# Performance work log

Hardware: AMD Instinct MI355X
Metric: run time of the kernel (lower is better)

## Reference

```python
import jax, jax.numpy as jnp
import numpy as np

EPS = 1e-8  # torch F.cosine_similarity norm clamp


def setup_inputs() -> dict:
    key = jax.random.key(0)
    ks = jax.random.split(key, 5)
    B, H, C, S, CS, K = 256, 256, 16384, 64, 32, 8
    query = jax.random.normal(ks[0], (B, H), dtype=jnp.float32)
    episode_embeddings = jax.random.normal(ks[1], (C, H), dtype=jnp.float32)
    episodes = jax.random.normal(ks[2], (C, S, H), dtype=jnp.float32)
    compressed_episodes = jax.random.normal(ks[3], (C, CS, H), dtype=jnp.float32)
    is_compressed = jax.random.randint(ks[4], (C,), 0, 2) == 1
    return {
        "query": query,
        "episode_embeddings": episode_embeddings,
        "episodes": episodes,
        "compressed_episodes": compressed_episodes,
        "is_compressed": is_compressed,
        "k": K,
    }


def reference(query, episode_embeddings, episodes, compressed_episodes, is_compressed, k):
    # cosine similarity  [B, C]
    qn = query / jnp.maximum(jnp.linalg.norm(query, axis=-1, keepdims=True), EPS)
    en = episode_embeddings / jnp.maximum(
        jnp.linalg.norm(episode_embeddings, axis=-1, keepdims=True), EPS)
    sim = qn @ en.T
    top_scores, top_idx = jax.lax.top_k(sim, k)  # [B, k]

    S = episodes.shape[1]
    CS = compressed_episodes.shape[1]
    full = episodes[top_idx]                # [B, k, S, H] gather
    comp = compressed_episodes[top_idx]     # [B, k, CS, H] gather
    comp_padded = jnp.pad(comp, ((0, 0), (0, 0), (0, S - CS), (0, 0)))
    flag = is_compressed[top_idx][..., None, None]  # [B, k, 1, 1]
    retrieved = jnp.where(flag, comp_padded, full)  # [B, k, S, H]
    return retrieved, top_scores
```

## Files before the change

### kernel.cpp

```cpp
#include <hip/hip_runtime.h>
#include <math.h>

#define B_  256
#define H_  256
#define C_  16384
#define S_  64
#define CS_ 32
#define K_  8
#define EPS 1e-8f
#define RET_ ((size_t)B_ * K_ * S_ * H_)

typedef __attribute__((ext_vector_type(8))) short short8v;
typedef __attribute__((ext_vector_type(4))) float f32x4;


__device__ inline unsigned short f2bf(float f) {
    unsigned u = __builtin_bit_cast(unsigned, f);
    unsigned r = u + 0x7fffu + ((u >> 16) & 1u);
    return (unsigned short)(r >> 16);
}
__device__ inline unsigned ordf(float f) {
    unsigned u = __builtin_bit_cast(unsigned, f);
    return u ^ ((u >> 31) ? 0xFFFFFFFFu : 0x80000000u);
}
__device__ inline short8v pack8(float4 a, float4 b) {
    short8v r;
    r[0] = (short)f2bf(a.x); r[1] = (short)f2bf(a.y);
    r[2] = (short)f2bf(a.z); r[3] = (short)f2bf(a.w);
    r[4] = (short)f2bf(b.x); r[5] = (short)f2bf(b.y);
    r[6] = (short)f2bf(b.z); r[7] = (short)f2bf(b.w);
    return r;
}
__device__ inline void ce(unsigned long long& a, unsigned long long& b) {
    unsigned long long lo = a < b ? a : b;
    a = a < b ? b : a;
    b = lo;
}
__device__ inline void merge_shfl(unsigned long long best[8], int xorlane) {
    unsigned long long m[8];
    #pragma unroll
    for (int i = 0; i < 8; ++i) {
        unsigned long long p = __shfl_xor(best[7 - i], xorlane);
        m[i] = best[i] > p ? best[i] : p;
    }
    ce(m[0], m[4]); ce(m[1], m[5]); ce(m[2], m[6]); ce(m[3], m[7]);
    ce(m[0], m[2]); ce(m[1], m[3]); ce(m[4], m[6]); ce(m[5], m[7]);
    ce(m[0], m[1]); ce(m[2], m[3]); ce(m[4], m[5]); ce(m[6], m[7]);
    #pragma unroll
    for (int i = 0; i < 8; ++i) best[i] = m[i];
}

#define LSTR 40
__global__ __launch_bounds__(256) void simsel_kernel(const float* __restrict__ q,
                                                     const float* __restrict__ e,
                                                     const unsigned* __restrict__ icw,
                                                     unsigned long long* __restrict__ candbuf,
                                                     int* __restrict__ mode) {
    const int t = threadIdx.x;
    if (blockIdx.x == 1024) {
        __shared__ int f;
        if (t == 0) f = 0;
        __syncthreads();
        int any = 0;
        for (int i = t; i < 4096; i += 256)
            if (icw[i] & 0xFFFFFF00u) any = 1;
        if (any) atomicOr(&f, 1);
        __syncthreads();
        if (t == 0) *mode = f;
        return;
    }

    __shared__ union {
        struct { unsigned short Qs[64 * LSTR]; unsigned short Es[64 * LSTR]; } st;
        float tile[64 * 65];
    } sm;
    __shared__ float einv_s[64];
    const int lane = t & 63, wv = t >> 6;
    const int wm = wv >> 1, wn = wv & 1;
    const int bid = blockIdx.x;
    const int ct = (bid & 7) * 32 + (bid >> 5);
    const int bt = (bid >> 3) & 3;
    const int c0 = ct * 64, b0 = bt * 64;
    const int r = t >> 2, g = t & 3;
    const float4* q4 = (const float4*)q;
    const float4* e4 = (const float4*)e;

    float esq = 0.f;
    f32x4 acc[2][2];
    #pragma unroll
    for (int i = 0; i < 2; ++i)
        #pragma unroll
        for (int j = 0; j < 2; ++j) acc[i][j] = (f32x4){0.f, 0.f, 0.f, 0.f};

    for (int hc = 0; hc < 8; ++hc) {
        __syncthreads();
        float4 a0 = q4[(size_t)(b0 + r) * 64 + hc * 8 + g * 2];
        float4 a1 = q4[(size_t)(b0 + r) * 64 + hc * 8 + g * 2 + 1];
        float4 e0 = e4[(size_t)(c0 + r) * 64 + hc * 8 + g * 2];
        float4 e1 = e4[(size_t)(c0 + r) * 64 + hc * 8 + g * 2 + 1];
        esq += e0.x * e0.x + e0.y * e0.y + e0.z * e0.z + e0.w * e0.w
             + e1.x * e1.x + e1.y * e1.y + e1.z * e1.z + e1.w * e1.w;
        *(short8v*)&sm.st.Qs[r * LSTR + g * 8] = pack8(a0, a1);
        *(short8v*)&sm.st.Es[r * LSTR + g * 8] = pack8(e0, e1);
        __syncthreads();

        short8v afr[2], bfr[2];
        #pragma unroll
        for (int mi = 0; mi < 2; ++mi)
            afr[mi] = *(short8v*)&sm.st.Qs[(wm * 32 + mi * 16 + (lane & 15)) * LSTR + (lane >> 4) * 8];
        #pragma unroll
        for (int ni = 0; ni < 2; ++ni)
            bfr[ni] = *(short8v*)&sm.st.Es[(wn * 32 + ni * 16 + (lane & 15)) * LSTR + (lane >> 4) * 8];
        #pragma unroll
        for (int mi = 0; mi < 2; ++mi)
            #pragma unroll
            for (int ni = 0; ni < 2; ++ni)
                acc[mi][ni] = __builtin_amdgcn_mfma_f32_16x16x32_bf16(
                    afr[mi], bfr[ni], acc[mi][ni], 0, 0, 0);
    }

    esq += __shfl_xor(esq, 1);
    esq += __shfl_xor(esq, 2);
    if (g == 0) einv_s[r] = 1.0f / fmaxf(sqrtf(esq), EPS);
    __syncthreads();

    #pragma unroll
    for (int mi = 0; mi < 2; ++mi)
        #pragma unroll
        for (int j = 0; j < 4; ++j) {
            int row = wm * 32 + mi * 16 + (lane >> 4) * 4 + j;
            #pragma unroll
            for (int ni = 0; ni < 2; ++ni) {
                int col = wn * 32 + ni * 16 + (lane & 15);
                sm.tile[row * 65 + col] = acc[mi][ni][j] * einv_s[col];
            }
        }
    __syncthreads();

    unsigned long long best[8];
    #pragma unroll
    for (int k = 0; k < 8; ++k) best[k] = 0ull;
    for (int i = 0; i < 16; ++i) {
        int c = g * 16 + i;
        float v = sm.tile[r * 65 + c];
        unsigned long long key = ((unsigned long long)ordf(v) << 32)
                               | (unsigned)(0xFFFFFFFFu - (unsigned)(c0 + c));
        if (key > best[7]) {
            best[7] = key;
            #pragma unroll
            for (int k = 7; k > 0; --k)
                if (best[k] > best[k - 1]) {
                    unsigned long long tmp = best[k];
                    best[k] = best[k - 1]; best[k - 1] = tmp;
                }
        }
    }
    merge_shfl(best, 1);
    merge_shfl(best, 2);
    if (g == 0) {
        #pragma unroll
        for (int k = 0; k < 8; ++k)
            candbuf[(size_t)(b0 + r) * 2048 + ct * 8 + k] = best[k];
    }
}

__global__ __launch_bounds__(256) void merge_kernel(const float* __restrict__ q,
                                                    const float* __restrict__ e,
                                                    const unsigned long long* __restrict__ candbuf,
                                                    float* __restrict__ out_scores,
                                                    int* __restrict__ top_idx) {
    __shared__ unsigned long long wtop[4][32];
    __shared__ unsigned long long sel32[32];
    __shared__ float rs[32];
    __shared__ int   ri[32];
    const int t = threadIdx.x, b = blockIdx.x;
    const int wv = t >> 6, lane = t & 63;

    const unsigned long long* lp = candbuf + (size_t)b * 2048 + (size_t)(wv * 64 + lane) * 8;
    unsigned long long k0 = lp[0], k1 = lp[1], k2 = lp[2], k3 = lp[3],
                       k4 = lp[4], k5 = lp[5], k6 = lp[6], k7 = lp[7];
    int p = 0;
    unsigned long long cur = k0;

    for (int it = 0; it < 32; ++it) {
        unsigned long long km = cur;
        #pragma unroll
        for (int d = 1; d < 64; d <<= 1) {
            unsigned long long o = __shfl_xor(km, d);
            km = o > km ? o : km;
        }
        if (lane == 0) wtop[wv][it] = km;
        if (cur == km) {
            ++p;
            cur = (p == 1) ? k1 : (p == 2) ? k2 : (p == 3) ? k3 : (p == 4) ? k4
                : (p == 5) ? k5 : (p == 6) ? k6 : (p == 7) ? k7 : 0ull;
        }
    }
    __syncthreads();

    if (t == 0) {
        int i0 = 0, i1 = 0, i2 = 0, i3 = 0;
        for (int it = 0; it < 32; ++it) {
            unsigned long long v0 = (i0 < 32) ? wtop[0][i0] : 0ull;
            unsigned long long v1 = (i1 < 32) ? wtop[1][i1] : 0ull;
            unsigned long long v2 = (i2 < 32) ? wtop[2][i2] : 0ull;
            unsigned long long v3 = (i3 < 32) ? wtop[3][i3] : 0ull;
            unsigned long long m01 = v0 > v1 ? v0 : v1;
            unsigned long long m23 = v2 > v3 ? v2 : v3;
            unsigned long long mx  = m01 > m23 ? m01 : m23;
            sel32[it] = mx;
            if (mx == v0) ++i0; else if (mx == v1) ++i1;
            else if (mx == v2) ++i2; else ++i3;
        }
    }
    __syncthreads();

    float4 qv = ((const float4*)q)[(size_t)b * 64 + lane];
    float qsq = qv.x * qv.x + qv.y * qv.y + qv.z * qv.z + qv.w * qv.w;
    #pragma unroll
    for (int d = 1; d < 64; d <<= 1) qsq += __shfl_xor(qsq, d);
    float qi = 1.0f / fmaxf(sqrtf(qsq), EPS);

    for (int m = wv; m < 32; m += 4) {
        int idx = (int)(0xFFFFFFFFu - (unsigned)(sel32[m] & 0xFFFFFFFFull));
        float4 ev = ((const float4*)e)[(size_t)idx * 64 + lane];
        float dot = qv.x * ev.x + qv.y * ev.y + qv.z * ev.z + qv.w * ev.w;
        float ss  = ev.x * ev.x + ev.y * ev.y + ev.z * ev.z + ev.w * ev.w;
        #pragma unroll
        for (int d = 1; d < 64; d <<= 1) {
            dot += __shfl_xor(dot, d);
            ss  += __shfl_xor(ss, d);
        }
        if (lane == 0) {
            rs[m] = dot * qi * (1.0f / fmaxf(sqrtf(ss), EPS));
            ri[m] = idx;
        }
    }
    __syncthreads();

    if (t < 64) {
        float val; int idx, slot;
        if (t < 32) { val = rs[t]; idx = ri[t]; slot = t; }
        else        { val = -INFINITY; idx = 0x7fffffff; slot = -1; }
        for (int pp = 0; pp < 8; ++pp) {
            float bs = val; int bi = idx, bsl = slot;
            #pragma unroll
            for (int d = 1; d < 64; d <<= 1) {
                float os = __shfl_xor(bs, d);
                int   oi = __shfl_xor(bi, d);
                int   osl = __shfl_xor(bsl, d);
                if (os > bs || (os == bs && oi < bi)) { bs = os; bi = oi; bsl = osl; }
            }
            if (t == 0) { out_scores[b * K_ + pp] = bs; top_idx[b * K_ + pp] = bi; }
            if (slot == bsl) val = -INFINITY;
        }
    }
}

__global__ __launch_bounds__(256) void gather_kernel(const float* __restrict__ epi,
                                                     const float* __restrict__ comp,
                                                     const void* __restrict__ icp,
                                                     const int* __restrict__ top_idx,
                                                     const int* __restrict__ mode,
                                                     float* __restrict__ out) {
    const int bj = blockIdx.x;
    const int c = top_idx[bj];
    const int m = *mode;
    const int flag = m ? (((const unsigned char*)icp)[c] != 0)
                       : (((const int*)icp)[c] != 0);
    const int t = threadIdx.x;
    f32x4* o4 = (f32x4*)out + (size_t)bj * 4096;
    if (!flag) {
        const f32x4* s4 = (const f32x4*)epi + (size_t)c * 4096;
        #pragma unroll 4
        for (int i = t; i < 4096; i += 256)
            __builtin_nontemporal_store(__builtin_nontemporal_load(s4 + i), o4 + i);
    } else {
        const f32x4* s4 = (const f32x4*)comp + (size_t)c * 2048;
        #pragma unroll 4
        for (int i = t; i < 2048; i += 256)
            __builtin_nontemporal_store(__builtin_nontemporal_load(s4 + i), o4 + i);
        const f32x4 z = (f32x4){0.f, 0.f, 0.f, 0.f};
        #pragma unroll 4
        for (int i = 2048 + t; i < 4096; i += 256)
            __builtin_nontemporal_store(z, o4 + i);
    }
}

extern "C" void kernel_launch(void* const* d_in, const int* in_sizes, int n_in,
                              void* d_out, int out_size, void* d_ws, size_t ws_size,
                              hipStream_t stream) {
    const float* query = (const float*)d_in[0];
    const float* emb   = (const float*)d_in[1];
    const float* epi   = (const float*)d_in[2];
    const float* comp  = (const float*)d_in[3];
    const void*  icp   = d_in[4];
    float* out = (float*)d_out;

    unsigned long long* candbuf = (unsigned long long*)d_ws;
    int* mode   = (int*)((char*)d_ws + (4u << 20));
    int* topidx = mode + 1;
    float* out_scores = out + RET_;

    simsel_kernel<<<1025, 256, 0, stream>>>(query, emb, (const unsigned*)icp,
                                            candbuf, mode);
    merge_kernel<<<B_, 256, 0, stream>>>(query, emb, candbuf, out_scores, topidx);
    gather_kernel<<<B_ * K_, 256, 0, stream>>>(epi, comp, icp, topidx, mode, out);
}
```

Measured before the change: 107.6 us.

## Fuse merge into gather with redundant per-block selection; double-buffer simsel loads

Merges the top-k merge and gather kernels into one launch in which each (batch, slot) block recomputes the full candidate merge and then copies its selected episode. This removes a kernel launch and the top_idx round trip, at the cost of eight times the merge work and candidate-buffer reads. The similarity kernel now processes 64-wide K chunks with register prefetch of the next chunk, halving the barrier count and overlapping global loads with MFMA work. The shared-memory row stride is widened to fit the larger chunk.

```diff
diff --git a/kernel.cpp b/kernel.cpp
--- a/kernel.cpp
+++ b/kernel.cpp
@@ -50,7 +50,7 @@
     for (int i = 0; i < 8; ++i) best[i] = m[i];
 }
 
-#define LSTR 40
+#define LSTR 72
 __global__ __launch_bounds__(256) void simsel_kernel(const float* __restrict__ q,
                                                      const float* __restrict__ e,
                                                      const unsigned* __restrict__ icw,
@@ -92,31 +92,53 @@
         #pragma unroll
         for (int j = 0; j < 2; ++j) acc[i][j] = (f32x4){0.f, 0.f, 0.f, 0.f};
 
-    for (int hc = 0; hc < 8; ++hc) {
+    float4 qb[2][4], eb[2][4];
+    #pragma unroll
+    for (int u = 0; u < 4; ++u) {
+        qb[0][u] = q4[(size_t)(b0 + r) * 64 + g * 4 + u];
+        eb[0][u] = e4[(size_t)(c0 + r) * 64 + g * 4 + u];
+    }
+
+    #pragma unroll
+    for (int hc = 0; hc < 4; ++hc) {
+        const int cur = hc & 1, nxt = cur ^ 1;
+        #pragma unroll
+        for (int u = 0; u < 4; ++u) {
+            float4 ev = eb[cur][u];
+            esq += ev.x * ev.x + ev.y * ev.y + ev.z * ev.z + ev.w * ev.w;
+        }
+        *(short8v*)&sm.st.Qs[r * LSTR + g * 16]     = pack8(qb[cur][0], qb[cur][1]);
+        *(short8v*)&sm.st.Qs[r * LSTR + g * 16 + 8] = pack8(qb[cur][2], qb[cur][3]);
+        *(short8v*)&sm.st.Es[r * LSTR + g * 16]     = pack8(eb[cur][0], eb[cur][1]);
+        *(short8v*)&sm.st.Es[r * LSTR + g * 16 + 8] = pack8(eb[cur][2], eb[cur][3]);
+        if (hc < 3) {
+            #pragma unroll
+            for (int u = 0; u < 4; ++u) {
+                qb[nxt][u] = q4[(size_t)(b0 + r) * 64 + (hc + 1) * 16 + g * 4 + u];
+                eb[nxt][u] = e4[(size_t)(c0 + r) * 64 + (hc + 1) * 16 + g * 4 + u];
+            }
+        }
         __syncthreads();
-        float4 a0 = q4[(size_t)(b0 + r) * 64 + hc * 8 + g * 2];
-        float4 a1 = q4[(size_t)(b0 + r) * 64 + hc * 8 + g * 2 + 1];
-        float4 e0 = e4[(size_t)(c0 + r) * 64 + hc * 8 + g * 2];
-        float4 e1 = e4[(size_t)(c0 + r) * 64 + hc * 8 + g * 2 + 1];
-        esq += e0.x * e0.x + e0.y * e0.y + e0.z * e0.z + e0.w * e0.w
-             + e1.x * e1.x + e1.y * e1.y + e1.z * e1.z + e1.w * e1.w;
-        *(short8v*)&sm.st.Qs[r * LSTR + g * 8] = pack8(a0, a1);
-        *(short8v*)&sm.st.Es[r * LSTR + g * 8] = pack8(e0, e1);
+
+        #pragma unroll
+        for (int ks = 0; ks < 2; ++ks) {
+            short8v afr[2], bfr[2];
+            #pragma unroll
+            for (int mi = 0; mi < 2; ++mi)
+                afr[mi] = *(short8v*)&sm.st.Qs[(wm * 32 + mi * 16 + (lane & 15)) * LSTR
+                                               + ks * 32 + (lane >> 4) * 8];
+            #pragma unroll
+            for (int ni = 0; ni < 2; ++ni)
+                bfr[ni] = *(short8v*)&sm.st.Es[(wn * 32 + ni * 16 + (lane & 15)) * LSTR
+                                               + ks * 32 + (lane >> 4) * 8];
+            #pragma unroll
+            for (int mi = 0; mi < 2; ++mi)
+                #pragma unroll
+                for (int ni = 0; ni < 2; ++ni)
+                    acc[mi][ni] = __builtin_amdgcn_mfma_f32_16x16x32_bf16(
+                        afr[mi], bfr[ni], acc[mi][ni], 0, 0, 0);
+        }
         __syncthreads();
-
-        short8v afr[2], bfr[2];
-        #pragma unroll
-        for (int mi = 0; mi < 2; ++mi)
-            afr[mi] = *(short8v*)&sm.st.Qs[(wm * 32 + mi * 16 + (lane & 15)) * LSTR + (lane >> 4) * 8];
-        #pragma unroll
-        for (int ni = 0; ni < 2; ++ni)
-            bfr[ni] = *(short8v*)&sm.st.Es[(wn * 32 + ni * 16 + (lane & 15)) * LSTR + (lane >> 4) * 8];
-        #pragma unroll
-        for (int mi = 0; mi < 2; ++mi)
-            #pragma unroll
-            for (int ni = 0; ni < 2; ++ni)
-                acc[mi][ni] = __builtin_amdgcn_mfma_f32_16x16x32_bf16(
-                    afr[mi], bfr[ni], acc[mi][ni], 0, 0, 0);
     }
 
     esq += __shfl_xor(esq, 1);
@@ -164,16 +186,19 @@
     }
 }
 
-__global__ __launch_bounds__(256) void merge_kernel(const float* __restrict__ q,
-                                                    const float* __restrict__ e,
-                                                    const unsigned long long* __restrict__ candbuf,
-                                                    float* __restrict__ out_scores,
-                                                    int* __restrict__ top_idx) {
+__global__ __launch_bounds__(256) void merge_gather_kernel(
+        const float* __restrict__ q, const float* __restrict__ e,
+        const unsigned long long* __restrict__ candbuf,
+        const void* __restrict__ icp, const int* __restrict__ mode,
+        const float* __restrict__ epi, const float* __restrict__ comp,
+        float* __restrict__ out, float* __restrict__ out_scores) {
     __shared__ unsigned long long wtop[4][32];
     __shared__ unsigned long long sel32[32];
     __shared__ float rs[32];
     __shared__ int   ri[32];
-    const int t = threadIdx.x, b = blockIdx.x;
+    __shared__ int   sel_c;
+    const int t = threadIdx.x;
+    const int j = blockIdx.x >> 8, b = blockIdx.x & 255;
     const int wv = t >> 6, lane = t & 63;
 
     const unsigned long long* lp = candbuf + (size_t)b * 2048 + (size_t)(wv * 64 + lane) * 8;
@@ -251,25 +276,17 @@
                 int   osl = __shfl_xor(bsl, d);
                 if (os > bs || (os == bs && oi < bi)) { bs = os; bi = oi; bsl = osl; }
             }
-            if (t == 0) { out_scores[b * K_ + pp] = bs; top_idx[b * K_ + pp] = bi; }
+            if (t == 0 && pp == j) { out_scores[b * K_ + j] = bs; sel_c = bi; }
             if (slot == bsl) val = -INFINITY;
         }
     }
-}
-
-__global__ __launch_bounds__(256) void gather_kernel(const float* __restrict__ epi,
-                                                     const float* __restrict__ comp,
-                                                     const void* __restrict__ icp,
-                                                     const int* __restrict__ top_idx,
-                                                     const int* __restrict__ mode,
-                                                     float* __restrict__ out) {
-    const int bj = blockIdx.x;
-    const int c = top_idx[bj];
-    const int m = *mode;
-    const int flag = m ? (((const unsigned char*)icp)[c] != 0)
-                       : (((const int*)icp)[c] != 0);
-    const int t = threadIdx.x;
-    f32x4* o4 = (f32x4*)out + (size_t)bj * 4096;
+    __syncthreads();
+
+    const int c = sel_c;
+    const int m_ = *mode;
+    const int flag = m_ ? (((const unsigned char*)icp)[c] != 0)
+                        : (((const int*)icp)[c] != 0);
+    f32x4* o4 = (f32x4*)out + ((size_t)b * K_ + j) * 4096;
     if (!flag) {
         const f32x4* s4 = (const f32x4*)epi + (size_t)c * 4096;
         #pragma unroll 4
@@ -298,12 +315,11 @@
     float* out = (float*)d_out;
 
     unsigned long long* candbuf = (unsigned long long*)d_ws;
-    int* mode   = (int*)((char*)d_ws + (4u << 20));
-    int* topidx = mode + 1;
+    int* mode = (int*)((char*)d_ws + (4u << 20));
     float* out_scores = out + RET_;
 
     simsel_kernel<<<1025, 256, 0, stream>>>(query, emb, (const unsigned*)icp,
                                             candbuf, mode);
-    merge_kernel<<<B_, 256, 0, stream>>>(query, emb, candbuf, out_scores, topidx);
-    gather_kernel<<<B_ * K_, 256, 0, stream>>>(epi, comp, icp, topidx, mode, out);
-}
+    merge_gather_kernel<<<B_ * K_, 256, 0, stream>>>(query, emb, candbuf, icp, mode,
+                                                     epi, comp, out, out_scores);
+}
```

New measurement: 121.8 us. 1.13x slower.

## Double-buffer similarity GEMM smem tiles and parallelize top-k merge with bitonic shuffles

Applied to the files above, without the earlier changes.

The similarity kernel now double-buffers the Q and E shared-memory tiles. The next H-chunk is prefetched into registers while MFMAs run on the current one, which removes one barrier per iteration. In the merge kernel, the serial single-thread 4-way merge of per-wave top-32 lists is replaced by two stages of bitonic-merge shuffles across wavefronts. This costs more shared memory and register pressure in exchange for latency hiding and less serial work.

```diff
diff --git a/kernel.cpp b/kernel.cpp
--- a/kernel.cpp
+++ b/kernel.cpp
@@ -71,7 +71,7 @@
     }
 
     __shared__ union {
-        struct { unsigned short Qs[64 * LSTR]; unsigned short Es[64 * LSTR]; } st;
+        unsigned short st[4][64 * LSTR];
         float tile[64 * 65];
     } sm;
     __shared__ float einv_s[64];
@@ -92,31 +92,48 @@
         #pragma unroll
         for (int j = 0; j < 2; ++j) acc[i][j] = (f32x4){0.f, 0.f, 0.f, 0.f};
 
+    {
+        float4 qa0 = q4[(size_t)(b0 + r) * 64 + g * 2];
+        float4 qa1 = q4[(size_t)(b0 + r) * 64 + g * 2 + 1];
+        float4 ea0 = e4[(size_t)(c0 + r) * 64 + g * 2];
+        float4 ea1 = e4[(size_t)(c0 + r) * 64 + g * 2 + 1];
+        esq += ea0.x * ea0.x + ea0.y * ea0.y + ea0.z * ea0.z + ea0.w * ea0.w
+             + ea1.x * ea1.x + ea1.y * ea1.y + ea1.z * ea1.z + ea1.w * ea1.w;
+        *(short8v*)&sm.st[0][r * LSTR + g * 8] = pack8(qa0, qa1);
+        *(short8v*)&sm.st[2][r * LSTR + g * 8] = pack8(ea0, ea1);
+    }
+
     for (int hc = 0; hc < 8; ++hc) {
+        const int cur = hc & 1, nxt = cur ^ 1;
+        float4 qa0, qa1, ea0, ea1;
+        if (hc < 7) {
+            qa0 = q4[(size_t)(b0 + r) * 64 + (hc + 1) * 8 + g * 2];
+            qa1 = q4[(size_t)(b0 + r) * 64 + (hc + 1) * 8 + g * 2 + 1];
+            ea0 = e4[(size_t)(c0 + r) * 64 + (hc + 1) * 8 + g * 2];
+            ea1 = e4[(size_t)(c0 + r) * 64 + (hc + 1) * 8 + g * 2 + 1];
+        }
         __syncthreads();
-        float4 a0 = q4[(size_t)(b0 + r) * 64 + hc * 8 + g * 2];
-        float4 a1 = q4[(size_t)(b0 + r) * 64 + hc * 8 + g * 2 + 1];
-        float4 e0 = e4[(size_t)(c0 + r) * 64 + hc * 8 + g * 2];
-        float4 e1 = e4[(size_t)(c0 + r) * 64 + hc * 8 + g * 2 + 1];
-        esq += e0.x * e0.x + e0.y * e0.y + e0.z * e0.z + e0.w * e0.w
-             + e1.x * e1.x + e1.y * e1.y + e1.z * e1.z + e1.w * e1.w;
-        *(short8v*)&sm.st.Qs[r * LSTR + g * 8] = pack8(a0, a1);
-        *(short8v*)&sm.st.Es[r * LSTR + g * 8] = pack8(e0, e1);
-        __syncthreads();
 
         short8v afr[2], bfr[2];
         #pragma unroll
         for (int mi = 0; mi < 2; ++mi)
-            afr[mi] = *(short8v*)&sm.st.Qs[(wm * 32 + mi * 16 + (lane & 15)) * LSTR + (lane >> 4) * 8];
+            afr[mi] = *(short8v*)&sm.st[cur][(wm * 32 + mi * 16 + (lane & 15)) * LSTR + (lane >> 4) * 8];
         #pragma unroll
         for (int ni = 0; ni < 2; ++ni)
-            bfr[ni] = *(short8v*)&sm.st.Es[(wn * 32 + ni * 16 + (lane & 15)) * LSTR + (lane >> 4) * 8];
+            bfr[ni] = *(short8v*)&sm.st[2 + cur][(wn * 32 + ni * 16 + (lane & 15)) * LSTR + (lane >> 4) * 8];
         #pragma unroll
         for (int mi = 0; mi < 2; ++mi)
             #pragma unroll
             for (int ni = 0; ni < 2; ++ni)
                 acc[mi][ni] = __builtin_amdgcn_mfma_f32_16x16x32_bf16(
                     afr[mi], bfr[ni], acc[mi][ni], 0, 0, 0);
+
+        if (hc < 7) {
+            esq += ea0.x * ea0.x + ea0.y * ea0.y + ea0.z * ea0.z + ea0.w * ea0.w
+                 + ea1.x * ea1.x + ea1.y * ea1.y + ea1.z * ea1.z + ea1.w * ea1.w;
+            *(short8v*)&sm.st[nxt][r * LSTR + g * 8] = pack8(qa0, qa1);
+            *(short8v*)&sm.st[2 + nxt][r * LSTR + g * 8] = pack8(ea0, ea1);
+        }
     }
 
     esq += __shfl_xor(esq, 1);
@@ -170,6 +187,7 @@
                                                     float* __restrict__ out_scores,
                                                     int* __restrict__ top_idx) {
     __shared__ unsigned long long wtop[4][32];
+    __shared__ unsigned long long m2[2][32];
     __shared__ unsigned long long sel32[32];
     __shared__ float rs[32];
     __shared__ int   ri[32];
@@ -198,20 +216,25 @@
     }
     __syncthreads();
 
-    if (t == 0) {
-        int i0 = 0, i1 = 0, i2 = 0, i3 = 0;
-        for (int it = 0; it < 32; ++it) {
-            unsigned long long v0 = (i0 < 32) ? wtop[0][i0] : 0ull;
-            unsigned long long v1 = (i1 < 32) ? wtop[1][i1] : 0ull;
-            unsigned long long v2 = (i2 < 32) ? wtop[2][i2] : 0ull;
-            unsigned long long v3 = (i3 < 32) ? wtop[3][i3] : 0ull;
-            unsigned long long m01 = v0 > v1 ? v0 : v1;
-            unsigned long long m23 = v2 > v3 ? v2 : v3;
-            unsigned long long mx  = m01 > m23 ? m01 : m23;
-            sel32[it] = mx;
-            if (mx == v0) ++i0; else if (mx == v1) ++i1;
-            else if (mx == v2) ++i2; else ++i3;
-        }
+    if (wv < 2) {
+        unsigned long long v = (lane < 32) ? wtop[2 * wv][lane]
+                                           : wtop[2 * wv + 1][63 - lane];
+        #pragma unroll
+        for (int d = 32; d > 0; d >>= 1) {
+            unsigned long long o = __shfl_xor(v, d);
+            v = ((lane & d) == 0) ? (v > o ? v : o) : (v < o ? v : o);
+        }
+        if (lane < 32) m2[wv][lane] = v;
+    }
+    __syncthreads();
+    if (wv == 0) {
+        unsigned long long v = (lane < 32) ? m2[0][lane] : m2[1][63 - lane];
+        #pragma unroll
+        for (int d = 32; d > 0; d >>= 1) {
+            unsigned long long o = __shfl_xor(v, d);
+            v = ((lane & d) == 0) ? (v > o ? v : o) : (v < o ? v : o);
+        }
+        if (lane < 32) sel32[lane] = v;
     }
     __syncthreads();
 
```

Measured after the change: 104.0 us. -3.4%, faster.
